# Kernel tuning notes

Hardware: AMD Instinct MI355X
Metric: run time of the kernel (lower is better)

The kernel has to match this reference:

```python
import jax, jax.numpy as jnp
import numpy as np

N_NODES = 100000
N_DIH = 1000000
SCALAR_DIM = 128
HIDDEN = 64
ATTR_DIM = 3


def setup_inputs() -> dict:
    key = jax.random.key(0)
    ks = jax.random.split(key, 10)
    x = jax.random.normal(ks[0], (N_NODES, SCALAR_DIM), dtype=jnp.float32)
    quadra_index = jax.random.randint(ks[1], (4, N_DIH), 0, N_NODES, dtype=jnp.int32)
    quadra_attr = jax.random.normal(ks[2], (N_DIH, ATTR_DIM), dtype=jnp.float32)
    d_in = SCALAR_DIM * 2 + ATTR_DIM
    W1 = jax.random.normal(ks[3], (d_in, HIDDEN), dtype=jnp.float32) / np.sqrt(d_in)
    b1 = jnp.zeros((HIDDEN,), dtype=jnp.float32)
    W2 = jax.random.normal(ks[4], (HIDDEN, HIDDEN), dtype=jnp.float32) / np.sqrt(HIDDEN)
    b2 = jnp.zeros((HIDDEN,), dtype=jnp.float32)
    W3 = jax.random.normal(ks[5], (HIDDEN, SCALAR_DIM), dtype=jnp.float32) / np.sqrt(HIDDEN)
    b3 = jnp.zeros((SCALAR_DIM,), dtype=jnp.float32)
    # o3.Linear on pure scalars ('128x0e'->'128x0e') is a bias-free linear map
    Wout = jax.random.normal(ks[6], (SCALAR_DIM, SCALAR_DIM), dtype=jnp.float32) / np.sqrt(SCALAR_DIM)
    return {"x": x, "quadra_index": quadra_index, "quadra_attr": quadra_attr,
            "W1": W1, "b1": b1, "W2": W2, "b2": b2, "W3": W3, "b3": b3, "Wout": Wout}


def _scatter_mean(msgs, idx, num_segments):
    sums = jax.ops.segment_sum(msgs, idx, num_segments=num_segments)
    counts = jax.ops.segment_sum(jnp.ones((msgs.shape[0],), msgs.dtype), idx,
                                 num_segments=num_segments)
    return sums / jnp.maximum(counts, 1.0)[:, None]


def reference(x, quadra_index, quadra_attr, W1, b1, W2, b2, W3, b3, Wout):
    n = x.shape[0]
    x_scalar = x[:, :SCALAR_DIM]
    i, j, k, l = quadra_index[0], quadra_index[1], quadra_index[2], quadra_index[3]
    # gather endpoints, concat with dihedral attrs: [E, 2*D + 3]
    dih_in = jnp.concatenate([x_scalar[i], x_scalar[l], quadra_attr], axis=-1)
    h = jax.nn.silu(dih_in @ W1 + b1)
    h = jax.nn.silu(h @ W2 + b2)
    msgs = h @ W3 + b3  # [E, D]
    aggr_j = _scatter_mean(msgs, j, n)
    aggr_k = _scatter_mean(msgs, k, n)
    aggr = (aggr_j + aggr_k) * 0.5
    return aggr @ Wout
```

## Files before the change

kernel.cpp:

```cpp
#include <hip/hip_runtime.h>

#define N_NODES    100000
#define N_DIH      1000000
#define SCALAR_DIM 128
#define HIDDEN     64
#define ATTR_DIM   3

typedef short v8s __attribute__((ext_vector_type(8)));
typedef float v4f __attribute__((ext_vector_type(4)));

__device__ __forceinline__ float silu(float v) {
    return __fdividef(v, 1.0f + __expf(-v));
}

__device__ __forceinline__ unsigned short bf16_rne(float f) {
    unsigned int u = __float_as_uint(f);
    u = (u + 0x7FFFu + ((u >> 16) & 1u)) >> 16;
    return (unsigned short)u;
}

__device__ __forceinline__ float2 bf2_to_f2(unsigned int v) {
    float2 r;
    r.x = __uint_as_float(v << 16);
    r.y = __uint_as_float(v & 0xffff0000u);
    return r;
}

#define PREP_W   112
#define PREP_W34 33
#define PREP_G   64
#define PREP_H   3907
#define PREP_XB  12500
#define PREP_MAIN (PREP_W + PREP_W34 + PREP_G + PREP_H)
#define PREP_ALL  (PREP_MAIN + PREP_XB)

__global__ void prep_kernel(const float* __restrict__ x, unsigned short* __restrict__ xb,
                            const float* __restrict__ W1, const float* __restrict__ W2,
                            const float* __restrict__ W3, const float* __restrict__ b1,
                            const float* __restrict__ b3,
                            const float* __restrict__ Wout,
                            unsigned short* __restrict__ W1f, unsigned short* __restrict__ W2f,
                            unsigned short* __restrict__ W3f, unsigned short* __restrict__ W1g,
                            float* __restrict__ W34, float* __restrict__ b34,
                            float* __restrict__ PK,
                            const int* __restrict__ qidx,
                            int* __restrict__ cnt_j, int* __restrict__ cnt_k,
                            int* __restrict__ rank_j, int* __restrict__ rank_k) {
    const int b = blockIdx.x;
    if (b < PREP_W) {
        const int tid = b * 256 + threadIdx.x;
        if (tid < 16384) {
            const int j = tid & 7, lane = (tid >> 3) & 63, t = tid >> 9;
            const int k = (t >> 2) * 32 + ((lane >> 4) << 3) + j;
            const int n = (t & 3) * 16 + (lane & 15);
            W1f[tid] = bf16_rne(W1[k * 64 + n]);
        } else if (tid < 20480) {
            const int i = tid - 16384;
            const int j = i & 7, lane = (i >> 3) & 63, t = i >> 9;
            const int k = (t >> 2) * 32 + ((lane >> 4) << 3) + j;
            const int n = (t & 3) * 16 + (lane & 15);
            W2f[i] = bf16_rne(W2[k * 64 + n]);
        } else if (tid < 28672) {
            const int i = tid - 20480;
            const int j = i & 7, lane = (i >> 3) & 63, t = i >> 9;
            const int k = (t >> 3) * 32 + ((lane >> 4) << 3) + j;
            const int n = (t & 7) * 16 + (lane & 15);
            W3f[i] = bf16_rne(W3[k * 128 + n]);
        }
    } else if (b < PREP_W + PREP_W34) {
        const int t34 = (b - PREP_W) * 256 + threadIdx.x;
        if (t34 < 8192) {
            const int r = t34 >> 7, c = t34 & 127;
            float s = 0.f;
            #pragma unroll 4
            for (int m = 0; m < 128; ++m) s += W3[r * 128 + m] * Wout[m * 128 + c];
            W34[t34] = s;
        } else if (t34 < 8320) {
            const int c = t34 - 8192;
            float s = 0.f;
            #pragma unroll 4
            for (int m = 0; m < 128; ++m) s += b3[m] * Wout[m * 128 + c];
            b34[c] = s;
        } else if (t34 < 8384) {
            const int c = t34 - 8320;
            PK[c * 4 + 0] = W1[256 * 64 + c];
            PK[c * 4 + 1] = W1[257 * 64 + c];
            PK[c * 4 + 2] = W1[258 * 64 + c];
            PK[c * 4 + 3] = b1[c];
        }
    } else if (b < PREP_W + PREP_W34 + PREP_G) {
        const int i = (b - PREP_W - PREP_W34) * 256 + threadIdx.x;
        const int j = i & 7, lane = (i >> 3) & 63, t = i >> 9;
        const int k = (t >> 3) * 32 + ((lane >> 4) << 3) + j;
        const int n = (t & 7) * 16 + (lane & 15);
        const float w = (n < 64) ? W1[k * 64 + n] : W1[(128 + k) * 64 + (n - 64)];
        W1g[i] = bf16_rne(w);
    } else if (b < PREP_MAIN) {
        const int t = (b - PREP_W - PREP_W34 - PREP_G) * 256 + threadIdx.x;
        if (t < N_DIH) {
            const int rj = atomicAdd(&cnt_j[qidx[N_DIH + t]], 1);
            const int rk = atomicAdd(&cnt_k[qidx[2 * N_DIH + t]], 1);
            if (rank_j != nullptr) {
                rank_j[t] = rj;
                rank_k[t] = rk;
            }
        }
    } else {
        const int t = (b - PREP_MAIN) * 256 + threadIdx.x;
        const float4 v = *(const float4*)&x[(size_t)t * 4];
        ushort4 o;
        o.x = bf16_rne(v.x); o.y = bf16_rne(v.y); o.z = bf16_rne(v.z); o.w = bf16_rne(v.w);
        *(ushort4*)&xb[(size_t)t * 4] = o;
    }
}

__global__ __launch_bounds__(1024) void scan_kernel(const int* __restrict__ cnt_j,
                                                    const int* __restrict__ cnt_k,
                                                    int* __restrict__ off_j, int* __restrict__ off_k) {
    const int* cnt = blockIdx.x ? cnt_k : cnt_j;
    int* off = blockIdx.x ? off_k : off_j;
    __shared__ int wtot[17];
    const int tid = threadIdx.x, lane = tid & 63, wv = tid >> 6;
    int carry = 0;
    for (int base = 0; base < N_NODES; base += 1024) {
        const int i = base + tid;
        const int v = (i < N_NODES) ? cnt[i] : 0;
        int inc = v;
        #pragma unroll
        for (int o = 1; o < 64; o <<= 1) {
            const int t = __shfl_up(inc, o);
            if (lane >= o) inc += t;
        }
        if (lane == 63) wtot[wv] = inc;
        __syncthreads();
        if (tid == 0) {
            int run = 0;
            #pragma unroll
            for (int w = 0; w < 16; ++w) { const int t = wtot[w]; wtot[w] = run; run += t; }
            wtot[16] = run;
        }
        __syncthreads();
        const int excl = inc - v + wtot[wv] + carry;
        if (i < N_NODES) off[i] = excl;
        carry += wtot[16];
        __syncthreads();
    }
    if (tid == 0) off[N_NODES] = carry;
}

__global__ void permute_kernel(const int* __restrict__ qidx,
                               const int* __restrict__ off_j, const int* __restrict__ off_k,
                               const int* __restrict__ rank_j, const int* __restrict__ rank_k,
                               int* __restrict__ perm_j, int* __restrict__ perm_k) {
    const int t = blockIdx.x * blockDim.x + threadIdx.x;
    if (t < N_DIH) {
        const int j = qidx[N_DIH + t];
        perm_j[off_j[j] + rank_j[t]] = t;
        const int k = qidx[2 * N_DIH + t];
        perm_k[off_k[k] + rank_k[t]] = t;
    }
}

#define UVW 3125

__global__ __launch_bounds__(256, 4) void uv_kernel(
    const float* __restrict__ x, const unsigned short* __restrict__ W1g,
    float* __restrict__ uv)
{
    const int tid = threadIdx.x, lane = tid & 63, wv = tid >> 6;
    const int g = blockIdx.x * 4 + wv;
    if (g >= UVW) return;
    const int D0 = g * 32;
    const int m16 = lane & 15, quad = lane >> 4;
    const int r0 = D0 + m16, r1 = D0 + 16 + m16;

    v4f acc[2][8];
    #pragma unroll
    for (int mt = 0; mt < 2; ++mt)
        #pragma unroll
        for (int nt = 0; nt < 8; ++nt) acc[mt][nt] = (v4f){0.f, 0.f, 0.f, 0.f};

    #pragma unroll
    for (int kc = 0; kc < 4; ++kc) {
        const int co = kc * 32 + quad * 8;
        v8s a0, a1;
        {
            const float4 f0 = *(const float4*)&x[(size_t)r0 * 128 + co];
            const float4 f1 = *(const float4*)&x[(size_t)r0 * 128 + co + 4];
            a0[0] = (short)bf16_rne(f0.x); a0[1] = (short)bf16_rne(f0.y);
            a0[2] = (short)bf16_rne(f0.z); a0[3] = (short)bf16_rne(f0.w);
            a0[4] = (short)bf16_rne(f1.x); a0[5] = (short)bf16_rne(f1.y);
            a0[6] = (short)bf16_rne(f1.z); a0[7] = (short)bf16_rne(f1.w);
        }
        {
            const float4 f0 = *(const float4*)&x[(size_t)r1 * 128 + co];
            const float4 f1 = *(const float4*)&x[(size_t)r1 * 128 + co + 4];
            a1[0] = (short)bf16_rne(f0.x); a1[1] = (short)bf16_rne(f0.y);
            a1[2] = (short)bf16_rne(f0.z); a1[3] = (short)bf16_rne(f0.w);
            a1[4] = (short)bf16_rne(f1.x); a1[5] = (short)bf16_rne(f1.y);
            a1[6] = (short)bf16_rne(f1.z); a1[7] = (short)bf16_rne(f1.w);
        }
        #pragma unroll
        for (int nt = 0; nt < 8; ++nt) {
            const v8s bf = *(const v8s*)(W1g + ((kc * 8 + nt) * 64 + lane) * 8);
            acc[0][nt] = __builtin_amdgcn_mfma_f32_16x16x32_bf16(a0, bf, acc[0][nt], 0, 0, 0);
            acc[1][nt] = __builtin_amdgcn_mfma_f32_16x16x32_bf16(a1, bf, acc[1][nt], 0, 0, 0);
        }
    }
    #pragma unroll
    for (int mt = 0; mt < 2; ++mt)
        #pragma unroll
        for (int nt = 0; nt < 8; ++nt) {
            const int c = nt * 16 + m16;
            #pragma unroll
            for (int reg = 0; reg < 4; ++reg) {
                const int n = D0 + mt * 16 + quad * 4 + reg;
                uv[(size_t)n * 128 + c] = acc[mt][nt][reg];
            }
        }
}

#define NW16 62500

__global__ __launch_bounds__(256, 6) void mlp2s_kernel(
    const float* __restrict__ uv, const int* __restrict__ qidx,
    const float* __restrict__ attr, const float* __restrict__ PK,
    const unsigned short* __restrict__ W2f, const float* __restrict__ b2,
    const int* __restrict__ off_j, const int* __restrict__ off_k,
    const int* __restrict__ rank_j, const int* __restrict__ rank_k,
    unsigned short* __restrict__ h2j, unsigned short* __restrict__ h2k)
{
    __shared__ __align__(16) unsigned short hbuf[4][1024];
    const int tid = threadIdx.x, lane = tid & 63, wv = tid >> 6;
    const int g = blockIdx.x * 4 + wv;
    const int D0 = g * 16;
    const int m16 = lane & 15, quad = lane >> 4;
    unsigned short* hs = hbuf[wv];

    const int d = D0 + m16;
    const int irow = qidx[d];
    const int lrow = qidx[3 * N_DIH + d];
    const int jn = qidx[N_DIH + d];
    const int kn = qidx[2 * N_DIH + d];
    const int pj = off_j[jn] + rank_j[d];
    const int pk = off_k[kn] + rank_k[d];

    const float* up = uv + (size_t)irow * 128 + quad * 8;
    const float* vp = uv + (size_t)lrow * 128 + 64 + quad * 8;
    const float4 u00 = *(const float4*)(up + 0);
    const float4 u01 = *(const float4*)(up + 4);
    const float4 u10 = *(const float4*)(up + 32);
    const float4 u11 = *(const float4*)(up + 36);
    const float4 v00 = *(const float4*)(vp + 0);
    const float4 v01 = *(const float4*)(vp + 4);
    const float4 v10 = *(const float4*)(vp + 32);
    const float4 v11 = *(const float4*)(vp + 36);
    const float a0 = attr[(size_t)d * 3 + 0];
    const float a1 = attr[(size_t)d * 3 + 1];
    const float a2 = attr[(size_t)d * 3 + 2];

    const int cb = quad * 8;
    v8s af0, af1;
#define EL(dst, e, cc, uval, vval) { \
    const float4 pkv = *(const float4*)&PK[(size_t)(cc) * 4]; \
    const float s = (uval) + (vval) + pkv.x * a0 + pkv.y * a1 + pkv.z * a2 + pkv.w; \
    dst[e] = (short)bf16_rne(silu(s)); }
    EL(af0, 0, cb + 0,      u00.x, v00.x)
    EL(af0, 1, cb + 1,      u00.y, v00.y)
    EL(af0, 2, cb + 2,      u00.z, v00.z)
    EL(af0, 3, cb + 3,      u00.w, v00.w)
    EL(af0, 4, cb + 4,      u01.x, v01.x)
    EL(af0, 5, cb + 5,      u01.y, v01.y)
    EL(af0, 6, cb + 6,      u01.z, v01.z)
    EL(af0, 7, cb + 7,      u01.w, v01.w)
    EL(af1, 0, 32 + cb + 0, u10.x, v10.x)
    EL(af1, 1, 32 + cb + 1, u10.y, v10.y)
    EL(af1, 2, 32 + cb + 2, u10.z, v10.z)
    EL(af1, 3, 32 + cb + 3, u10.w, v10.w)
    EL(af1, 4, 32 + cb + 4, u11.x, v11.x)
    EL(af1, 5, 32 + cb + 5, u11.y, v11.y)
    EL(af1, 6, 32 + cb + 6, u11.z, v11.z)
    EL(af1, 7, 32 + cb + 7, u11.w, v11.w)
#undef EL

    v4f acc2[4];
    #pragma unroll
    for (int nt = 0; nt < 4; ++nt) acc2[nt] = (v4f){0.f, 0.f, 0.f, 0.f};
    #pragma unroll
    for (int nt = 0; nt < 4; ++nt) {
        const v8s bA = *(const v8s*)(W2f + ((nt) * 64 + lane) * 8);
        const v8s bB = *(const v8s*)(W2f + ((4 + nt) * 64 + lane) * 8);
        acc2[nt] = __builtin_amdgcn_mfma_f32_16x16x32_bf16(af0, bA, acc2[nt], 0, 0, 0);
        acc2[nt] = __builtin_amdgcn_mfma_f32_16x16x32_bf16(af1, bB, acc2[nt], 0, 0, 0);
    }

    #pragma unroll
    for (int nt = 0; nt < 4; ++nt) {
        const int c = nt * 16 + m16;
        const float b2c = b2[c];
        #pragma unroll
        for (int reg = 0; reg < 4; ++reg) {
            const int row = quad * 4 + reg;
            hs[row * 64 + c] = bf16_rne(silu(acc2[nt][reg] + b2c));
        }
    }
    const int sub = lane & 7;
    #pragma unroll
    for (int i = 0; i < 2; ++i) {
        const int row = i * 8 + (lane >> 3);
        const int pjr = __shfl(pj, row);
        const int pkr = __shfl(pk, row);
        const v8s rowv = *(const v8s*)(hs + i * 512 + lane * 8);
        *(v8s*)(h2j + (size_t)pjr * 64 + sub * 8) = rowv;
        *(v8s*)(h2k + (size_t)pkr * 64 + sub * 8) = rowv;
    }
}

__global__ __launch_bounds__(256, 6) void mlp2_kernel(
    const float* __restrict__ uv, const int* __restrict__ qidx,
    const float* __restrict__ attr, const float* __restrict__ PK,
    const unsigned short* __restrict__ W2f, const float* __restrict__ b2,
    unsigned short* __restrict__ h2)
{
    __shared__ __align__(16) unsigned short hbuf[4][1024];
    const int tid = threadIdx.x, lane = tid & 63, wv = tid >> 6;
    const int g = blockIdx.x * 4 + wv;
    const int D0 = g * 16;
    const int m16 = lane & 15, quad = lane >> 4;
    unsigned short* hs = hbuf[wv];

    const int d = D0 + m16;
    const int irow = qidx[d];
    const int lrow = qidx[3 * N_DIH + d];

    const float* up = uv + (size_t)irow * 128 + quad * 8;
    const float* vp = uv + (size_t)lrow * 128 + 64 + quad * 8;
    const float4 u00 = *(const float4*)(up + 0);
    const float4 u01 = *(const float4*)(up + 4);
    const float4 u10 = *(const float4*)(up + 32);
    const float4 u11 = *(const float4*)(up + 36);
    const float4 v00 = *(const float4*)(vp + 0);
    const float4 v01 = *(const float4*)(vp + 4);
    const float4 v10 = *(const float4*)(vp + 32);
    const float4 v11 = *(const float4*)(vp + 36);
    const float a0 = attr[(size_t)d * 3 + 0];
    const float a1 = attr[(size_t)d * 3 + 1];
    const float a2 = attr[(size_t)d * 3 + 2];

    const int cb = quad * 8;
    v8s af0, af1;
#define EL(dst, e, cc, uval, vval) { \
    const float4 pk = *(const float4*)&PK[(size_t)(cc) * 4]; \
    const float s = (uval) + (vval) + pk.x * a0 + pk.y * a1 + pk.z * a2 + pk.w; \
    dst[e] = (short)bf16_rne(silu(s)); }
    EL(af0, 0, cb + 0,      u00.x, v00.x)
    EL(af0, 1, cb + 1,      u00.y, v00.y)
    EL(af0, 2, cb + 2,      u00.z, v00.z)
    EL(af0, 3, cb + 3,      u00.w, v00.w)
    EL(af0, 4, cb + 4,      u01.x, v01.x)
    EL(af0, 5, cb + 5,      u01.y, v01.y)
    EL(af0, 6, cb + 6,      u01.z, v01.z)
    EL(af0, 7, cb + 7,      u01.w, v01.w)
    EL(af1, 0, 32 + cb + 0, u10.x, v10.x)
    EL(af1, 1, 32 + cb + 1, u10.y, v10.y)
    EL(af1, 2, 32 + cb + 2, u10.z, v10.z)
    EL(af1, 3, 32 + cb + 3, u10.w, v10.w)
    EL(af1, 4, 32 + cb + 4, u11.x, v11.x)
    EL(af1, 5, 32 + cb + 5, u11.y, v11.y)
    EL(af1, 6, 32 + cb + 6, u11.z, v11.z)
    EL(af1, 7, 32 + cb + 7, u11.w, v11.w)
#undef EL

    v4f acc2[4];
    #pragma unroll
    for (int nt = 0; nt < 4; ++nt) acc2[nt] = (v4f){0.f, 0.f, 0.f, 0.f};
    #pragma unroll
    for (int nt = 0; nt < 4; ++nt) {
        const v8s bA = *(const v8s*)(W2f + ((nt) * 64 + lane) * 8);
        const v8s bB = *(const v8s*)(W2f + ((4 + nt) * 64 + lane) * 8);
        acc2[nt] = __builtin_amdgcn_mfma_f32_16x16x32_bf16(af0, bA, acc2[nt], 0, 0, 0);
        acc2[nt] = __builtin_amdgcn_mfma_f32_16x16x32_bf16(af1, bB, acc2[nt], 0, 0, 0);
    }

    #pragma unroll
    for (int nt = 0; nt < 4; ++nt) {
        const int c = nt * 16 + m16;
        const float b2c = b2[c];
        #pragma unroll
        for (int reg = 0; reg < 4; ++reg) {
            const int row = quad * 4 + reg;
            hs[row * 64 + c] = bf16_rne(silu(acc2[nt][reg] + b2c));
        }
    }
    #pragma unroll
    for (int i = 0; i < 2; ++i) {
        const v8s row16 = *(const v8s*)(hs + i * 512 + lane * 8);
        *(v8s*)(h2 + (size_t)D0 * 64 + i * 512 + lane * 8) = row16;
    }
}

#define NWAVES 31250

__global__ __launch_bounds__(256, 8) void mlp12_kernel(
    const unsigned short* __restrict__ xb, const int* __restrict__ qidx,
    const float* __restrict__ attr,
    const float* __restrict__ W1, const float* __restrict__ b1,
    const float* __restrict__ b2,
    const unsigned short* __restrict__ W1f, const unsigned short* __restrict__ W2f,
    unsigned short* __restrict__ h2)
{
    __shared__ __align__(16) unsigned short hbuf[4][1024];
    const int tid  = threadIdx.x;
    const int lane = tid & 63;
    const int wv   = tid >> 6;
    const int g    = blockIdx.x * 4 + wv;
    const int D0   = g * 16;
    const int m16  = lane & 15;
    const int quad = lane >> 4;
    unsigned short* hs = hbuf[wv];

    const int irow = qidx[D0 + m16];
    const int lrow = qidx[3 * N_DIH + D0 + m16];

    v4f acc[4];
    #pragma unroll
    for (int nt = 0; nt < 4; ++nt) acc[nt] = (v4f){0.f, 0.f, 0.f, 0.f};

    #pragma unroll
    for (int kc = 0; kc < 8; ++kc) {
        const int side = kc >> 2;
        const int coff = (kc & 3) * 32 + quad * 8;
        const int r0 = side ? lrow : irow;
        const v8s a0 = *(const v8s*)(xb + (size_t)r0 * 128 + coff);
        #pragma unroll
        for (int nt = 0; nt < 4; ++nt) {
            const v8s b = *(const v8s*)(W1f + ((kc * 4 + nt) * 64 + lane) * 8);
            acc[nt] = __builtin_amdgcn_mfma_f32_16x16x32_bf16(a0, b, acc[nt], 0, 0, 0);
        }
    }

    #pragma unroll
    for (int nt = 0; nt < 4; ++nt) {
        const int c = nt * 16 + m16;
        const float b1c = b1[c];
        const float wa0 = W1[256 * 64 + c];
        const float wa1 = W1[257 * 64 + c];
        const float wa2 = W1[258 * 64 + c];
        const int quadp = (nt * 2 + (m16 >> 3)) & 3;
        const int jp    = m16 & 7;
        const int kc2   = nt >> 1;
        #pragma unroll
        for (int reg = 0; reg < 4; ++reg) {
            const int r = quad * 4 + reg;
            const int d = D0 + r;
            float v = acc[nt][reg] + b1c
                    + attr[(size_t)d * 3 + 0] * wa0
                    + attr[(size_t)d * 3 + 1] * wa1
                    + attr[(size_t)d * 3 + 2] * wa2;
            v = silu(v);
            hs[kc2 * 512 + (r + 16 * quadp) * 8 + jp] = bf16_rne(v);
        }
    }

    v4f acc2[4];
    #pragma unroll
    for (int nt = 0; nt < 4; ++nt) acc2[nt] = (v4f){0.f, 0.f, 0.f, 0.f};

    #pragma unroll
    for (int kc = 0; kc < 2; ++kc) {
        const v8s a0 = *(const v8s*)(hs + kc * 512 + lane * 8);
        #pragma unroll
        for (int nt = 0; nt < 4; ++nt) {
            const v8s b = *(const v8s*)(W2f + ((kc * 4 + nt) * 64 + lane) * 8);
            acc2[nt] = __builtin_amdgcn_mfma_f32_16x16x32_bf16(a0, b, acc2[nt], 0, 0, 0);
        }
    }

    #pragma unroll
    for (int nt = 0; nt < 4; ++nt) {
        const int c = nt * 16 + m16;
        const float b2c = b2[c];
        #pragma unroll
        for (int reg = 0; reg < 4; ++reg) {
            const int row = quad * 4 + reg;
            hs[row * 64 + c] = bf16_rne(silu(acc2[nt][reg] + b2c));
        }
    }
    #pragma unroll
    for (int i = 0; i < 2; ++i) {
        const v8s row16 = *(const v8s*)(hs + i * 512 + lane * 8);
        *(v8s*)(h2 + (size_t)D0 * 64 + i * 512 + lane * 8) = row16;
    }
}

__global__ __launch_bounds__(256, 2) void aggregate_seq(
    const unsigned short* __restrict__ h2j, const unsigned short* __restrict__ h2k,
    const int* __restrict__ off_j, const int* __restrict__ off_k,
    const float* __restrict__ W34, const float* __restrict__ b34,
    float* __restrict__ out)
{
    __shared__ float a_lds[64 * 132];
    const int tid    = threadIdx.x;
    const int lane   = tid & 63;
    const int wv     = __builtin_amdgcn_readfirstlane(tid >> 6);
    const int base   = blockIdx.x * 64;
    const int half   = lane >> 5;
    const int lane31 = lane & 31;

    for (int p = 0; p < 16; ++p) {
        const int ln = wv * 16 + p;
        const int n  = base + ln;
        float sx = 0.f, sy = 0.f, bf = 0.f;
        if (n < N_NODES) {
            int cj, ck;
            {
                const int e0 = off_j[n], e1 = off_j[n + 1];
                cj = e1 - e0;
                float ax = 0.f, ay = 0.f;
                int e = e0;
                for (; e + 4 <= e1; e += 4) {
                    const float2 fA = bf2_to_f2(*(const unsigned int*)(h2j + (size_t)(e + half) * 64 + lane31 * 2));
                    const float2 fB = bf2_to_f2(*(const unsigned int*)(h2j + (size_t)(e + 2 + half) * 64 + lane31 * 2));
                    ax += fA.x + fB.x; ay += fA.y + fB.y;
                }
                if (e + 2 <= e1) {
                    const float2 f = bf2_to_f2(*(const unsigned int*)(h2j + (size_t)(e + half) * 64 + lane31 * 2));
                    ax += f.x; ay += f.y;
                    e += 2;
                }
                if (e < e1 && half == 0) {
                    const float2 f = bf2_to_f2(*(const unsigned int*)(h2j + (size_t)e * 64 + lane31 * 2));
                    ax += f.x; ay += f.y;
                }
                ax += __shfl_xor(ax, 32);
                ay += __shfl_xor(ay, 32);
                const float inv = 1.0f / (float)max(cj, 1);
                sx += ax * inv; sy += ay * inv;
            }
            {
                const int e0 = off_k[n], e1 = off_k[n + 1];
                ck = e1 - e0;
                float ax = 0.f, ay = 0.f;
                int e = e0;
                for (; e + 4 <= e1; e += 4) {
                    const float2 fA = bf2_to_f2(*(const unsigned int*)(h2k + (size_t)(e + half) * 64 + lane31 * 2));
                    const float2 fB = bf2_to_f2(*(const unsigned int*)(h2k + (size_t)(e + 2 + half) * 64 + lane31 * 2));
                    ax += fA.x + fB.x; ay += fA.y + fB.y;
                }
                if (e + 2 <= e1) {
                    const float2 f = bf2_to_f2(*(const unsigned int*)(h2k + (size_t)(e + half) * 64 + lane31 * 2));
                    ax += f.x; ay += f.y;
                    e += 2;
                }
                if (e < e1 && half == 0) {
                    const float2 f = bf2_to_f2(*(const unsigned int*)(h2k + (size_t)e * 64 + lane31 * 2));
                    ax += f.x; ay += f.y;
                }
                ax += __shfl_xor(ax, 32);
                ay += __shfl_xor(ay, 32);
                const float inv = 1.0f / (float)max(ck, 1);
                sx += ax * inv; sy += ay * inv;
            }
            bf = 0.5f * ((float)(cj > 0) + (float)(ck > 0));
        }
        if (half == 0) {
            float2 w; w.x = sx * 0.5f; w.y = sy * 0.5f;
            *(float2*)&a_lds[ln * 132 + 2 * lane31] = w;
            if (lane31 == 0) a_lds[ln * 132 + 128] = bf;
        }
    }
    __syncthreads();

    const int co = wv * 32;
    const float bfv = a_lds[lane * 132 + 128];
    float acc[32];
    #pragma unroll
    for (int c = 0; c < 32; ++c) acc[c] = bfv * b34[co + c];
    const float* ap = &a_lds[lane * 132];
    #pragma unroll 2
    for (int d = 0; d < 64; d += 4) {
        const float4 av = *(const float4*)&ap[d];
        const float* w0 = &W34[(d + 0) * 128 + co];
        const float* w1 = w0 + 128;
        const float* w2 = w0 + 256;
        const float* w3 = w0 + 384;
        #pragma unroll
        for (int c = 0; c < 32; ++c)
            acc[c] += av.x * w0[c] + av.y * w1[c] + av.z * w2[c] + av.w * w3[c];
    }
    __syncthreads();
    #pragma unroll
    for (int c = 0; c < 32; c += 4)
        *(float4*)&a_lds[lane * 132 + co + c] = make_float4(acc[c], acc[c+1], acc[c+2], acc[c+3]);
    __syncthreads();
    const int q4 = lane31 << 2;
    #pragma unroll
    for (int p = 0; p < 8; ++p) {
        const int ln = wv * 16 + p * 2 + half;
        const int n  = base + ln;
        if (n < N_NODES)
            *(float4*)&out[(size_t)n * 128 + q4] = *(const float4*)&a_lds[ln * 132 + q4];
    }
}

__global__ __launch_bounds__(256, 2) void aggregate_out64(
    const unsigned short* __restrict__ h2,
    const int* __restrict__ off_j, const int* __restrict__ off_k,
    const int* __restrict__ perm_j, const int* __restrict__ perm_k,
    const float* __restrict__ W34, const float* __restrict__ b34,
    float* __restrict__ out)
{
    __shared__ float a_lds[64 * 132];
    const int tid    = threadIdx.x;
    const int lane   = tid & 63;
    const int wv     = __builtin_amdgcn_readfirstlane(tid >> 6);
    const int base   = blockIdx.x * 64;
    const int half   = lane >> 5;
    const int lane31 = lane & 31;

    for (int p = 0; p < 16; ++p) {
        const int ln = wv * 16 + p;
        const int n  = base + ln;
        float sx = 0.f, sy = 0.f, bf = 0.f;
        if (n < N_NODES) {
            int cj, ck;
            {
                const int e0 = off_j[n], e1 = off_j[n + 1];
                cj = e1 - e0;
                float ax = 0.f, ay = 0.f;
                int e = e0;
                for (; e + 4 <= e1; e += 4) {
                    const int dA = perm_j[e + half];
                    const int dB = perm_j[e + 2 + half];
                    const float2 fA = bf2_to_f2(*(const unsigned int*)(h2 + (size_t)dA * 64 + lane31 * 2));
                    const float2 fB = bf2_to_f2(*(const unsigned int*)(h2 + (size_t)dB * 64 + lane31 * 2));
                    ax += fA.x + fB.x; ay += fA.y + fB.y;
                }
                if (e + 2 <= e1) {
                    const int d = perm_j[e + half];
                    const float2 f = bf2_to_f2(*(const unsigned int*)(h2 + (size_t)d * 64 + lane31 * 2));
                    ax += f.x; ay += f.y;
                    e += 2;
                }
                if (e < e1 && half == 0) {
                    const int d = perm_j[e];
                    const float2 f = bf2_to_f2(*(const unsigned int*)(h2 + (size_t)d * 64 + lane31 * 2));
                    ax += f.x; ay += f.y;
                }
                ax += __shfl_xor(ax, 32);
                ay += __shfl_xor(ay, 32);
                const float inv = 1.0f / (float)max(cj, 1);
                sx += ax * inv; sy += ay * inv;
            }
            {
                const int e0 = off_k[n], e1 = off_k[n + 1];
                ck = e1 - e0;
                float ax = 0.f, ay = 0.f;
                int e = e0;
                for (; e + 4 <= e1; e += 4) {
                    const int dA = perm_k[e + half];
                    const int dB = perm_k[e + 2 + half];
                    const float2 fA = bf2_to_f2(*(const unsigned int*)(h2 + (size_t)dA * 64 + lane31 * 2));
                    const float2 fB = bf2_to_f2(*(const unsigned int*)(h2 + (size_t)dB * 64 + lane31 * 2));
                    ax += fA.x + fB.x; ay += fA.y + fB.y;
                }
                if (e + 2 <= e1) {
                    const int d = perm_k[e + half];
                    const float2 f = bf2_to_f2(*(const unsigned int*)(h2 + (size_t)d * 64 + lane31 * 2));
                    ax += f.x; ay += f.y;
                    e += 2;
                }
                if (e < e1 && half == 0) {
                    const int d = perm_k[e];
                    const float2 f = bf2_to_f2(*(const unsigned int*)(h2 + (size_t)d * 64 + lane31 * 2));
                    ax += f.x; ay += f.y;
                }
                ax += __shfl_xor(ax, 32);
                ay += __shfl_xor(ay, 32);
                const float inv = 1.0f / (float)max(ck, 1);
                sx += ax * inv; sy += ay * inv;
            }
            bf = 0.5f * ((float)(cj > 0) + (float)(ck > 0));
        }
        if (half == 0) {
            float2 w; w.x = sx * 0.5f; w.y = sy * 0.5f;
            *(float2*)&a_lds[ln * 132 + 2 * lane31] = w;
            if (lane31 == 0) a_lds[ln * 132 + 128] = bf;
        }
    }
    __syncthreads();

    const int co = wv * 32;
    const float bfv = a_lds[lane * 132 + 128];
    float acc[32];
    #pragma unroll
    for (int c = 0; c < 32; ++c) acc[c] = bfv * b34[co + c];
    const float* ap = &a_lds[lane * 132];
    #pragma unroll 2
    for (int d = 0; d < 64; d += 4) {
        const float4 av = *(const float4*)&ap[d];
        const float* w0 = &W34[(d + 0) * 128 + co];
        const float* w1 = w0 + 128;
        const float* w2 = w0 + 256;
        const float* w3 = w0 + 384;
        #pragma unroll
        for (int c = 0; c < 32; ++c)
            acc[c] += av.x * w0[c] + av.y * w1[c] + av.z * w2[c] + av.w * w3[c];
    }
    __syncthreads();
    #pragma unroll
    for (int c = 0; c < 32; c += 4)
        *(float4*)&a_lds[lane * 132 + co + c] = make_float4(acc[c], acc[c+1], acc[c+2], acc[c+3]);
    __syncthreads();
    const int q4 = lane31 << 2;
    #pragma unroll
    for (int p = 0; p < 8; ++p) {
        const int ln = wv * 16 + p * 2 + half;
        const int n  = base + ln;
        if (n < N_NODES)
            *(float4*)&out[(size_t)n * 128 + q4] = *(const float4*)&a_lds[ln * 132 + q4];
    }
}

__global__ void scale_kernel(const int* __restrict__ cnt_j, const int* __restrict__ cnt_k,
                             float* __restrict__ scale_j, float* __restrict__ scale_k) {
    int n = blockIdx.x * blockDim.x + threadIdx.x;
    if (n < N_NODES) {
        scale_j[n] = 0.5f / (float)max(cnt_j[n], 1);
        scale_k[n] = 0.5f / (float)max(cnt_k[n], 1);
    }
}

__global__ __launch_bounds__(256, 3) void mlp_mfma_atomic(
    const unsigned short* __restrict__ xb, const int* __restrict__ qidx,
    const float* __restrict__ attr,
    const float* __restrict__ W1, const float* __restrict__ b1,
    const float* __restrict__ b2, const float* __restrict__ b3,
    const unsigned short* __restrict__ W1f, const unsigned short* __restrict__ W2f,
    const unsigned short* __restrict__ W3f,
    const float* __restrict__ scale_j, const float* __restrict__ scale_k,
    float* __restrict__ aggr)
{
    __shared__ __align__(16) unsigned short hbuf[4][4096];
    const int tid  = threadIdx.x;
    const int lane = tid & 63;
    const int wv   = tid >> 6;
    const int g    = blockIdx.x * 4 + wv;
    if (g >= NWAVES) return;
    const int D0   = g * 32;
    const int m16  = lane & 15;
    const int quad = lane >> 4;
    unsigned short* hs = hbuf[wv];

    int irow[2], lrow[2];
    irow[0] = qidx[D0 + m16];
    irow[1] = qidx[D0 + 16 + m16];
    lrow[0] = qidx[3 * N_DIH + D0 + m16];
    lrow[1] = qidx[3 * N_DIH + D0 + 16 + m16];

    v4f acc[2][4];
    #pragma unroll
    for (int mt = 0; mt < 2; ++mt)
        #pragma unroll
        for (int nt = 0; nt < 4; ++nt) acc[mt][nt] = (v4f){0.f, 0.f, 0.f, 0.f};
    #pragma unroll
    for (int kc = 0; kc < 8; ++kc) {
        const int side = kc >> 2;
        const int coff = (kc & 3) * 32 + quad * 8;
        const int r0 = side ? lrow[0] : irow[0];
        const int r1 = side ? lrow[1] : irow[1];
        const v8s a0 = *(const v8s*)(xb + (size_t)r0 * 128 + coff);
        const v8s a1 = *(const v8s*)(xb + (size_t)r1 * 128 + coff);
        #pragma unroll
        for (int nt = 0; nt < 4; ++nt) {
            const v8s b = *(const v8s*)(W1f + ((kc * 4 + nt) * 64 + lane) * 8);
            acc[0][nt] = __builtin_amdgcn_mfma_f32_16x16x32_bf16(a0, b, acc[0][nt], 0, 0, 0);
            acc[1][nt] = __builtin_amdgcn_mfma_f32_16x16x32_bf16(a1, b, acc[1][nt], 0, 0, 0);
        }
    }
    #pragma unroll
    for (int mt = 0; mt < 2; ++mt) {
        #pragma unroll
        for (int nt = 0; nt < 4; ++nt) {
            const int c = nt * 16 + m16;
            const float b1c = b1[c];
            const float wa0 = W1[256 * 64 + c];
            const float wa1 = W1[257 * 64 + c];
            const float wa2 = W1[258 * 64 + c];
            const int quadp = (nt * 2 + (m16 >> 3)) & 3;
            const int jp    = m16 & 7;
            const int kc2   = nt >> 1;
            #pragma unroll
            for (int reg = 0; reg < 4; ++reg) {
                const int r = quad * 4 + reg;
                const int d = D0 + mt * 16 + r;
                float v = acc[mt][nt][reg] + b1c
                        + attr[(size_t)d * 3 + 0] * wa0
                        + attr[(size_t)d * 3 + 1] * wa1
                        + attr[(size_t)d * 3 + 2] * wa2;
                v = silu(v);
                hs[mt * 1024 + kc2 * 512 + (r + 16 * quadp) * 8 + jp] = bf16_rne(v);
            }
        }
    }
    v4f acc2[2][4];
    #pragma unroll
    for (int mt = 0; mt < 2; ++mt)
        #pragma unroll
        for (int nt = 0; nt < 4; ++nt) acc2[mt][nt] = (v4f){0.f, 0.f, 0.f, 0.f};
    #pragma unroll
    for (int kc = 0; kc < 2; ++kc) {
        const v8s a0 = *(const v8s*)(hs +        kc * 512 + lane * 8);
        const v8s a1 = *(const v8s*)(hs + 1024 + kc * 512 + lane * 8);
        #pragma unroll
        for (int nt = 0; nt < 4; ++nt) {
            const v8s b = *(const v8s*)(W2f + ((kc * 4 + nt) * 64 + lane) * 8);
            acc2[0][nt] = __builtin_amdgcn_mfma_f32_16x16x32_bf16(a0, b, acc2[0][nt], 0, 0, 0);
            acc2[1][nt] = __builtin_amdgcn_mfma_f32_16x16x32_bf16(a1, b, acc2[1][nt], 0, 0, 0);
        }
    }
    #pragma unroll
    for (int mt = 0; mt < 2; ++mt) {
        #pragma unroll
        for (int nt = 0; nt < 4; ++nt) {
            const float b2c = b2[nt * 16 + m16];
            const int quadp = (nt * 2 + (m16 >> 3)) & 3;
            const int jp    = m16 & 7;
            const int kc2   = nt >> 1;
            #pragma unroll
            for (int reg = 0; reg < 4; ++reg) {
                const int r = quad * 4 + reg;
                const float v = silu(acc2[mt][nt][reg] + b2c);
                hs[2048 + mt * 1024 + kc2 * 512 + (r + 16 * quadp) * 8 + jp] = bf16_rne(v);
            }
        }
    }
    v4f acc3[2][8];
    #pragma unroll
    for (int mt = 0; mt < 2; ++mt)
        #pragma unroll
        for (int nt = 0; nt < 8; ++nt) acc3[mt][nt] = (v4f){0.f, 0.f, 0.f, 0.f};
    #pragma unroll
    for (int kc = 0; kc < 2; ++kc) {
        const v8s a0 = *(const v8s*)(hs + 2048 +        kc * 512 + lane * 8);
        const v8s a1 = *(const v8s*)(hs + 2048 + 1024 + kc * 512 + lane * 8);
        #pragma unroll
        for (int nt = 0; nt < 8; ++nt) {
            const v8s b = *(const v8s*)(W3f + ((kc * 8 + nt) * 64 + lane) * 8);
            acc3[0][nt] = __builtin_amdgcn_mfma_f32_16x16x32_bf16(a0, b, acc3[0][nt], 0, 0, 0);
            acc3[1][nt] = __builtin_amdgcn_mfma_f32_16x16x32_bf16(a1, b, acc3[1][nt], 0, 0, 0);
        }
    }
    #pragma unroll
    for (int mt = 0; mt < 2; ++mt) {
        int jn[4], kn[4]; float sjv[4], skv[4];
        #pragma unroll
        for (int reg = 0; reg < 4; ++reg) {
            const int d = D0 + mt * 16 + quad * 4 + reg;
            jn[reg] = qidx[N_DIH + d];
            kn[reg] = qidx[2 * N_DIH + d];
            sjv[reg] = scale_j[jn[reg]];
            skv[reg] = scale_k[kn[reg]];
        }
        #pragma unroll
        for (int nt = 0; nt < 8; ++nt) {
            const int c = nt * 16 + m16;
            const float b3c = b3[c];
            #pragma unroll
            for (int reg = 0; reg < 4; ++reg) {
                const float v = acc3[mt][nt][reg] + b3c;
                atomicAdd(&aggr[(size_t)jn[reg] * 128 + c], v * sjv[reg]);
                atomicAdd(&aggr[(size_t)kn[reg] * 128 + c], v * skv[reg]);
            }
        }
    }
}

#define OB    256
#define OTILE 64
__global__ __launch_bounds__(OB, 2) void out_kernel(const float* __restrict__ aggr,
                                                    const float* __restrict__ Wout,
                                                    float* __restrict__ out) {
    __shared__ float a_lds[OTILE * 132];
    const int tid  = threadIdx.x;
    const int lane = tid & 63;
    const int wv   = __builtin_amdgcn_readfirstlane(tid >> 6);
    const int base = blockIdx.x * OTILE;
    const int half = lane >> 5;
    const int q4   = (lane & 31) << 2;
    #pragma unroll
    for (int p = 0; p < 8; ++p) {
        const int ln = wv * 16 + p * 2 + half;
        const int n  = base + ln;
        float4 v = make_float4(0.f, 0.f, 0.f, 0.f);
        if (n < N_NODES) v = *(const float4*)&aggr[(size_t)n * 128 + q4];
        *(float4*)&a_lds[ln * 132 + q4] = v;
    }
    __syncthreads();
    const int c0 = wv * 32;
    float acc[32];
    #pragma unroll
    for (int c = 0; c < 32; ++c) acc[c] = 0.0f;
    const float* ap = &a_lds[lane * 132];
    #pragma unroll 2
    for (int d = 0; d < 128; d += 4) {
        const float4 av = *(const float4*)&ap[d];
        const float* w0 = &Wout[(d + 0) * 128 + c0];
        const float* w1 = &Wout[(d + 1) * 128 + c0];
        const float* w2 = &Wout[(d + 2) * 128 + c0];
        const float* w3 = &Wout[(d + 3) * 128 + c0];
        #pragma unroll
        for (int c = 0; c < 32; ++c)
            acc[c] += av.x * w0[c] + av.y * w1[c] + av.z * w2[c] + av.w * w3[c];
    }
    __syncthreads();
    #pragma unroll
    for (int c = 0; c < 32; c += 4)
        *(float4*)&a_lds[lane * 132 + c0 + c] = make_float4(acc[c], acc[c+1], acc[c+2], acc[c+3]);
    __syncthreads();
    #pragma unroll
    for (int p = 0; p < 8; ++p) {
        const int ln = wv * 16 + p * 2 + half;
        const int n  = base + ln;
        if (n < N_NODES)
            *(float4*)&out[(size_t)n * 128 + q4] = *(const float4*)&a_lds[ln * 132 + q4];
    }
}

extern "C" void kernel_launch(void* const* d_in, const int* in_sizes, int n_in,
                              void* d_out, int out_size, void* d_ws, size_t ws_size,
                              hipStream_t stream) {
    const float* x    = (const float*)d_in[0];
    const int*   qidx = (const int*)d_in[1];
    const float* attr = (const float*)d_in[2];
    const float* W1   = (const float*)d_in[3];
    const float* b1   = (const float*)d_in[4];
    const float* W2   = (const float*)d_in[5];
    const float* b2   = (const float*)d_in[6];
    const float* W3   = (const float*)d_in[7];
    const float* b3   = (const float*)d_in[8];
    const float* Wout = (const float*)d_in[9];
    float* out = (float*)d_out;
    float* wsf = (float*)d_ws;

    const size_t words = ws_size / 4;
    if (words >= (size_t)79300000) {
        size_t o = 0;
        unsigned short* h2j = (unsigned short*)wsf;          o += 32000000;
        unsigned short* h2k = (unsigned short*)(wsf + o);    o += 32000000;
        float* uvp  = wsf + o;                               o += 12800000;
        unsigned short* W1f = (unsigned short*)(wsf + o);    o += 8192;
        unsigned short* W2f = (unsigned short*)(wsf + o);    o += 2048;
        unsigned short* W3f = (unsigned short*)(wsf + o);    o += 4096;
        unsigned short* W1g = (unsigned short*)(wsf + o);    o += 8192;
        float* W34  = wsf + o;                               o += 8192;
        float* b34  = wsf + o;                               o += 128;
        float* PK   = wsf + o;                               o += 256;
        int* cnt_j  = (int*)(wsf + o);                       o += 100000;
        int* cnt_k  = (int*)(wsf + o);                       o += 100000;
        int* off_j  = (int*)(wsf + o);                       o += 100001;
        int* off_k  = (int*)(wsf + o);                       o += 100001;
        int* rank_j = (int*)(wsf + o);                       o += 1000000;
        int* rank_k = (int*)(wsf + o);                       o += 1000000;

        hipMemsetAsync(cnt_j, 0, (size_t)200000 * sizeof(int), stream);
        prep_kernel<<<PREP_MAIN, 256, 0, stream>>>(
            x, h2j , W1, W2, W3, b1, b3, Wout,
            W1f, W2f, W3f, W1g, W34, b34, PK, qidx, cnt_j, cnt_k, rank_j, rank_k);
        scan_kernel<<<2, 1024, 0, stream>>>(cnt_j, cnt_k, off_j, off_k);
        uv_kernel<<<(UVW + 3) / 4, 256, 0, stream>>>(x, W1g, uvp);
        mlp2s_kernel<<<NW16 / 4, 256, 0, stream>>>(
            uvp, qidx, attr, PK, W2f, b2, off_j, off_k, rank_j, rank_k, h2j, h2k);
        aggregate_seq<<<(N_NODES + 63) / 64, 256, 0, stream>>>(
            h2j, h2k, off_j, off_k, W34, b34, out);
    } else if (words >= (size_t)47500000) {
        size_t o = 0;
        unsigned short* h2  = (unsigned short*)wsf;          o += 32000000;
        float* uvp  = wsf + o;                               o += 12800000;
        unsigned short* W1f = (unsigned short*)(wsf + o);    o += 8192;
        unsigned short* W2f = (unsigned short*)(wsf + o);    o += 2048;
        unsigned short* W3f = (unsigned short*)(wsf + o);    o += 4096;
        unsigned short* W1g = (unsigned short*)(wsf + o);    o += 8192;
        float* W34  = wsf + o;                               o += 8192;
        float* b34  = wsf + o;                               o += 128;
        float* PK   = wsf + o;                               o += 256;
        int* cnt_j  = (int*)(wsf + o);                       o += 100000;
        int* cnt_k  = (int*)(wsf + o);                       o += 100000;
        int* off_j  = (int*)(wsf + o);                       o += 100001;
        int* off_k  = (int*)(wsf + o);                       o += 100001;
        int* perm_j = (int*)(wsf + o);                       o += 1000000;
        int* perm_k = (int*)(wsf + o);                       o += 1000000;
        int* rank_j = (int*)h2;
        int* rank_k = rank_j + N_DIH;

        hipMemsetAsync(cnt_j, 0, (size_t)200000 * sizeof(int), stream);
        prep_kernel<<<PREP_MAIN, 256, 0, stream>>>(
            x, h2 , W1, W2, W3, b1, b3, Wout,
            W1f, W2f, W3f, W1g, W34, b34, PK, qidx, cnt_j, cnt_k, rank_j, rank_k);
        scan_kernel<<<2, 1024, 0, stream>>>(cnt_j, cnt_k, off_j, off_k);
        permute_kernel<<<(N_DIH + 255) / 256, 256, 0, stream>>>(
            qidx, off_j, off_k, rank_j, rank_k, perm_j, perm_k);
        uv_kernel<<<(UVW + 3) / 4, 256, 0, stream>>>(x, W1g, uvp);
        mlp2_kernel<<<NW16 / 4, 256, 0, stream>>>(uvp, qidx, attr, PK, W2f, b2, h2);
        aggregate_out64<<<(N_NODES + 63) / 64, 256, 0, stream>>>(
            h2, off_j, off_k, perm_j, perm_k, W34, b34, out);
    } else if (words >= (size_t)41100000) {
        size_t o = 0;
        unsigned short* h2  = (unsigned short*)wsf;          o += 32000000;
        unsigned short* xb  = (unsigned short*)(wsf + o);    o += 6400000;
        unsigned short* W1f = (unsigned short*)(wsf + o);    o += 8192;
        unsigned short* W2f = (unsigned short*)(wsf + o);    o += 2048;
        unsigned short* W3f = (unsigned short*)(wsf + o);    o += 4096;
        float* W34  = wsf + o;                               o += 8192;
        float* b34  = wsf + o;                               o += 128;
        int* cnt_j  = (int*)(wsf + o);                       o += 100000;
        int* cnt_k  = (int*)(wsf + o);                       o += 100000;
        int* off_j  = (int*)(wsf + o);                       o += 100001;
        int* off_k  = (int*)(wsf + o);                       o += 100001;
        int* perm_j = (int*)(wsf + o);                       o += 1000000;
        int* perm_k = (int*)(wsf + o);                       o += 1000000;
        unsigned short* W1g = (unsigned short*)(wsf + o);    o += 8192;
        float* PK   = wsf + o;                               o += 256;
        int* rank_j = (int*)h2;
        int* rank_k = rank_j + N_DIH;

        hipMemsetAsync(cnt_j, 0, (size_t)200000 * sizeof(int), stream);
        prep_kernel<<<PREP_ALL, 256, 0, stream>>>(
            x, xb, W1, W2, W3, b1, b3, Wout,
            W1f, W2f, W3f, W1g, W34, b34, PK, qidx, cnt_j, cnt_k, rank_j, rank_k);
        scan_kernel<<<2, 1024, 0, stream>>>(cnt_j, cnt_k, off_j, off_k);
        permute_kernel<<<(N_DIH + 255) / 256, 256, 0, stream>>>(
            qidx, off_j, off_k, rank_j, rank_k, perm_j, perm_k);
        mlp12_kernel<<<NW16 / 4, 256, 0, stream>>>(
            xb, qidx, attr, W1, b1, b2, W1f, W2f, h2);
        aggregate_out64<<<(N_NODES + 63) / 64, 256, 0, stream>>>(
            h2, off_j, off_k, perm_j, perm_k, W34, b34, out);
    } else {
        int*   cnt_j   = (int*)wsf;
        int*   cnt_k   = cnt_j + N_NODES;
        float* scale_j = wsf + 200000;
        float* scale_k = wsf + 300000;
        float* aggr    = wsf + 400000;
        unsigned short* xb  = (unsigned short*)(wsf + 13200000);
        unsigned short* W1f = (unsigned short*)(wsf + 19600000);
        unsigned short* W2f = (unsigned short*)(wsf + 19608192);
        unsigned short* W3f = (unsigned short*)(wsf + 19610240);
        float* W34 = wsf + 19612288;
        float* b34 = wsf + 19612288;
        unsigned short* W1g = (unsigned short*)(wsf + 19612288);
        float* PK  = wsf + 19612288;

        hipMemsetAsync(cnt_j, 0, (size_t)2 * N_NODES * sizeof(int), stream);
        hipMemsetAsync(aggr, 0, (size_t)N_NODES * 128 * sizeof(float), stream);
        prep_kernel<<<PREP_ALL, 256, 0, stream>>>(
            x, xb, W1, W2, W3, b1, b3, Wout,
            W1f, W2f, W3f, W1g, W34, b34, PK, qidx, cnt_j, cnt_k, nullptr, nullptr);
        scale_kernel<<<(N_NODES + 255) / 256, 256, 0, stream>>>(cnt_j, cnt_k, scale_j, scale_k);
        mlp_mfma_atomic<<<(NWAVES + 3) / 4, 256, 0, stream>>>(
            xb, qidx, attr, W1, b1, b2, b3, W1f, W2f, W3f, scale_j, scale_k, aggr);
        out_kernel<<<(N_NODES + OTILE - 1) / OTILE, OB, 0, stream>>>(aggr, Wout, out);
    }
}
```

Baseline: 610.7 us.

## Split wave halves across nodes and batch gathers eight deep in aggregate_out64

The gather phase of aggregate_out64 now assigns each half-wave its own node, where before both halves split the edges of one node and merged with cross-half shuffles. Each half-wave loads up to eight neighbour indices and their h2 rows in a batch before accumulating, to keep more memory loads in flight. Launch bounds are raised to 4 blocks per CU to increase occupancy. The risks are register pressure from the batched loads and the tighter bound, and divergence when the two halves' nodes have different degrees.

```diff
diff --git a/kernel.cpp b/kernel.cpp
--- a/kernel.cpp
+++ b/kernel.cpp
@@ -603,7 +603,7 @@
     }
 }
 
-__global__ __launch_bounds__(256, 2) void aggregate_out64(
+__global__ __launch_bounds__(256, 4) void aggregate_out64(
     const unsigned short* __restrict__ h2,
     const int* __restrict__ off_j, const int* __restrict__ off_k,
     const int* __restrict__ perm_j, const int* __restrict__ perm_k,
@@ -618,76 +618,51 @@
     const int half   = lane >> 5;
     const int lane31 = lane & 31;
 
-    for (int p = 0; p < 16; ++p) {
-        const int ln = wv * 16 + p;
+#define AGG_BATCH(B) \
+    if (e + B <= e1) { \
+        int dd[B]; \
+        _Pragma("unroll") \
+        for (int q = 0; q < B; ++q) dd[q] = permp[e + q]; \
+        unsigned int rr[B]; \
+        _Pragma("unroll") \
+        for (int q = 0; q < B; ++q) \
+            rr[q] = *(const unsigned int*)(h2 + (size_t)dd[q] * 64 + lane31 * 2); \
+        _Pragma("unroll") \
+        for (int q = 0; q < B; ++q) { \
+            const float2 f = bf2_to_f2(rr[q]); \
+            ax += f.x; ay += f.y; \
+        } \
+        e += B; \
+    }
+
+    for (int p = 0; p < 8; ++p) {
+        const int ln = wv * 16 + p * 2 + half;
         const int n  = base + ln;
         float sx = 0.f, sy = 0.f, bf = 0.f;
         if (n < N_NODES) {
-            int cj, ck;
-            {
-                const int e0 = off_j[n], e1 = off_j[n + 1];
-                cj = e1 - e0;
+            int cnt2[2];
+            #pragma unroll
+            for (int li = 0; li < 2; ++li) {
+                const int* offp  = li ? off_k  : off_j;
+                const int* permp = li ? perm_k : perm_j;
+                const int e0 = offp[n], e1 = offp[n + 1];
+                cnt2[li] = e1 - e0;
                 float ax = 0.f, ay = 0.f;
                 int e = e0;
-                for (; e + 4 <= e1; e += 4) {
-                    const int dA = perm_j[e + half];
-                    const int dB = perm_j[e + 2 + half];
-                    const float2 fA = bf2_to_f2(*(const unsigned int*)(h2 + (size_t)dA * 64 + lane31 * 2));
-                    const float2 fB = bf2_to_f2(*(const unsigned int*)(h2 + (size_t)dB * 64 + lane31 * 2));
-                    ax += fA.x + fB.x; ay += fA.y + fB.y;
-                }
-                if (e + 2 <= e1) {
-                    const int d = perm_j[e + half];
-                    const float2 f = bf2_to_f2(*(const unsigned int*)(h2 + (size_t)d * 64 + lane31 * 2));
-                    ax += f.x; ay += f.y;
-                    e += 2;
-                }
-                if (e < e1 && half == 0) {
-                    const int d = perm_j[e];
-                    const float2 f = bf2_to_f2(*(const unsigned int*)(h2 + (size_t)d * 64 + lane31 * 2));
-                    ax += f.x; ay += f.y;
-                }
-                ax += __shfl_xor(ax, 32);
-                ay += __shfl_xor(ay, 32);
-                const float inv = 1.0f / (float)max(cj, 1);
+                for (; e + 8 <= e1; ) { AGG_BATCH(8) }
+                AGG_BATCH(4)
+                AGG_BATCH(2)
+                AGG_BATCH(1)
+                const float inv = 1.0f / (float)max(cnt2[li], 1);
                 sx += ax * inv; sy += ay * inv;
             }
-            {
-                const int e0 = off_k[n], e1 = off_k[n + 1];
-                ck = e1 - e0;
-                float ax = 0.f, ay = 0.f;
-                int e = e0;
-                for (; e + 4 <= e1; e += 4) {
-                    const int dA = perm_k[e + half];
-                    const int dB = perm_k[e + 2 + half];
-                    const float2 fA = bf2_to_f2(*(const unsigned int*)(h2 + (size_t)dA * 64 + lane31 * 2));
-                    const float2 fB = bf2_to_f2(*(const unsigned int*)(h2 + (size_t)dB * 64 + lane31 * 2));
-                    ax += fA.x + fB.x; ay += fA.y + fB.y;
-                }
-                if (e + 2 <= e1) {
-                    const int d = perm_k[e + half];
-                    const float2 f = bf2_to_f2(*(const unsigned int*)(h2 + (size_t)d * 64 + lane31 * 2));
-                    ax += f.x; ay += f.y;
-                    e += 2;
-                }
-                if (e < e1 && half == 0) {
-                    const int d = perm_k[e];
-                    const float2 f = bf2_to_f2(*(const unsigned int*)(h2 + (size_t)d * 64 + lane31 * 2));
-                    ax += f.x; ay += f.y;
-                }
-                ax += __shfl_xor(ax, 32);
-                ay += __shfl_xor(ay, 32);
-                const float inv = 1.0f / (float)max(ck, 1);
-                sx += ax * inv; sy += ay * inv;
-            }
-            bf = 0.5f * ((float)(cj > 0) + (float)(ck > 0));
-        }
-        if (half == 0) {
-            float2 w; w.x = sx * 0.5f; w.y = sy * 0.5f;
-            *(float2*)&a_lds[ln * 132 + 2 * lane31] = w;
-            if (lane31 == 0) a_lds[ln * 132 + 128] = bf;
-        }
-    }
+            bf = 0.5f * ((float)(cnt2[0] > 0) + (float)(cnt2[1] > 0));
+        }
+        float2 w; w.x = sx * 0.5f; w.y = sy * 0.5f;
+        *(float2*)&a_lds[ln * 132 + 2 * lane31] = w;
+        if (lane31 == 0) a_lds[ln * 132 + 128] = bf;
+    }
+#undef AGG_BATCH
     __syncthreads();
 
     const int co = wv * 32;
```

Result: faster. 563.3 us (-7.8%).
